# Performance work log

Measured on AMD Instinct MI355X. Metric: run time of the kernel, lower is better.

The kernel has to match this reference:

```python
import jax, jax.numpy as jnp
import numpy as np

N = 65536
R = 9          # num_relations + 1
D_IN = 256
D_HID = 512
D_OUT = 256
N_HIDDEN = 2


def _xavier(key, shape):
    fan_out, fan_in = shape[-2], shape[-1]
    limit = np.sqrt(6.0 / (fan_in + fan_out))
    return jax.random.uniform(key, shape, jnp.float32, -limit, limit)


def setup_inputs() -> dict:
    key = jax.random.key(0)
    ks = jax.random.split(key, 12)
    inp = {
        "x": jax.random.normal(ks[0], (N, D_IN), jnp.float32),
        "edge_attr": jax.random.uniform(ks[1], (N, R), jnp.float32),
    }
    dims = [(D_HID, D_IN)] + [(D_HID, D_HID)] * N_HIDDEN + [(D_OUT, D_HID)]
    for i, (o, ii) in enumerate(dims):
        inp[f"W{i}"] = _xavier(ks[2 + 2 * i], (R, o, ii))
        inp[f"b{i}"] = _xavier(ks[3 + 2 * i], (R, o))
    return inp


def _linear_kg(x, edge_attr, W, b):
    # roi,ni,nr->no : relation-mixed linear per node
    y = jnp.einsum("roi,ni,nr->no", W, x, edge_attr)
    return y + edge_attr @ b


def reference(x, edge_attr, W0, b0, W1, b1, W2, b2, W3, b3):
    y = jax.nn.relu(_linear_kg(x, edge_attr, W0, b0))
    y = jax.nn.relu(_linear_kg(y, edge_attr, W1, b1))
    y = jax.nn.relu(_linear_kg(y, edge_attr, W2, b2))
    y = _linear_kg(y, edge_attr, W3, b3)
    return y
```

## Files before the change

### kernel.cpp

```cpp
#include <hip/hip_runtime.h>
#include <stdint.h>

using f32x4  = __attribute__((ext_vector_type(4))) float;
using bf16x8 = __attribute__((ext_vector_type(8))) __bf16;

#define GLOAD_LDS16(src, dst) __builtin_amdgcn_global_load_lds(                 \
    (const __attribute__((address_space(1))) void*)(src),                      \
    (__attribute__((address_space(3))) void*)(dst), 16, 0, 0)


__global__ void cvt_x_kernel(const float* __restrict__ x, __bf16* __restrict__ out) {
    const int u    = blockIdx.x * 256 + threadIdx.x;
    const int lane = u & 63;
    const int f    = (u >> 6) & 31;
    const int c    = (u >> 11) & 1;
    const int rb   = u >> 12;
    const int row  = rb * 128 + ((f >> 2) << 4) + (lane & 15);
    const int i    = c * 128 + ((f & 3) << 5) + ((lane >> 4) << 3);
    const float4 a = *(const float4*)(x + (size_t)row * 256 + i);
    const float4 b = *(const float4*)(x + (size_t)row * 256 + i + 4);
    bf16x8 pv;
    pv[0] = (__bf16)a.x; pv[1] = (__bf16)a.y; pv[2] = (__bf16)a.z; pv[3] = (__bf16)a.w;
    pv[4] = (__bf16)b.x; pv[5] = (__bf16)b.y; pv[6] = (__bf16)b.z; pv[7] = (__bf16)b.w;
    *(bf16x8*)(out + (size_t)u * 8) = pv;
}

template<int I, int O>
__global__ void prep_w_kernel(const float* __restrict__ W, __bf16* __restrict__ Bt) {
    constexpr int NCH = I >> 7;
    const int u    = blockIdx.x * 256 + threadIdx.x;
    const int r    = blockIdx.y;
    const int nb   = blockIdx.z;
    const int lane = u & 63;
    const int g    = (u >> 6) & 15;
    const int h    = (u >> 10) & 1;
    const int c    = u >> 11;
    const int mi   = g >> 1;
    const int ks   = (h << 1) + (g & 1);
    const int row  = nb * 128 + mi * 16 + (lane & 15);
    const int i    = c * 128 + ks * 32 + ((lane >> 4) << 3);
    const float* src = W + ((size_t)r * O + row) * I + i;
    const float4 a = *(const float4*)src;
    const float4 b = *(const float4*)(src + 4);
    bf16x8 pv;
    pv[0] = (__bf16)a.x; pv[1] = (__bf16)a.y; pv[2] = (__bf16)a.z; pv[3] = (__bf16)a.w;
    pv[4] = (__bf16)b.x; pv[5] = (__bf16)b.y; pv[6] = (__bf16)b.z; pv[7] = (__bf16)b.w;
    *(bf16x8*)(Bt + ((((size_t)nb * 9 + r) * NCH + c) * 2048 + (u & 2047)) * 8) = pv;
}

template<int O>
__global__ void prep_bias_kernel(const float* __restrict__ b, __bf16* __restrict__ BtB) {
    const int u    = blockIdx.x * 256 + threadIdx.x;
    const int nb   = u >> 10;
    const int q    = u & 1023;
    const int lane = q & 63;
    const int f    = q >> 6;
    const int row  = nb * 128 + ((f >> 1) << 4) + (lane & 15);
    const int kb   = ((f & 1) << 5) + ((lane >> 4) << 3);
    bf16x8 pv;
#pragma unroll
    for (int e = 0; e < 8; ++e) {
        const int k = kb + e;
        pv[e] = (k < 9) ? (__bf16)b[(size_t)k * O + row] : (__bf16)0.f;
    }
    *(bf16x8*)(BtB + (size_t)u * 8) = pv;
}

template<int I, int O, bool RELU, bool OUTF32>
__global__ __launch_bounds__(256, 2)
void kg_gemm(const __bf16* __restrict__ A, const float* __restrict__ E,
             const __bf16* __restrict__ Bt, const __bf16* __restrict__ BtB,
             void* __restrict__ Outv) {
    constexpr int NCH = I >> 7;
    constexpr int NBN = O >> 7;
    static_assert((I & 127) == 0 && (O & 127) == 0, "tile divisibility");

    __shared__ __align__(16) char lds[4 * 16384 + 4608];
    float* const ldsE = (float*)(lds + 65536);

    const int tid  = threadIdx.x;
    const int nwg  = gridDim.x;
    const int braw = blockIdx.x;
    const int bid  = (braw & 7) * (nwg >> 3) + (braw >> 3);
    const int rb   = bid / NBN;
    const int nb   = bid % NBN;
    const int bm0  = rb << 7;
    const int bn0  = nb << 7;
    const int lane = tid & 63;
    const int wid  = tid >> 6;
    const int wr   = (wid >> 1) << 6;
    const int wc   = (wid & 1) << 6;
    const int l15  = lane & 15;
    const int lq   = lane >> 4;

    if (tid < 128) {
        const float* e = E + (size_t)(bm0 + tid) * 9;
#pragma unroll
        for (int q = 0; q < 9; ++q) ldsE[q * 128 + tid] = e[q];
    }
    asm volatile("s_waitcnt lgkmcnt(0)" ::: "memory");

    f32x4 acc[4][4];
#pragma unroll
    for (int m = 0; m < 4; ++m)
#pragma unroll
        for (int n = 0; n < 4; ++n)
            acc[m][n] = f32x4{0.f, 0.f, 0.f, 0.f};
    const f32x4 zero4 = {0.f, 0.f, 0.f, 0.f};

    const size_t Abase = (size_t)rb * NCH * 2048;
    const size_t Bbase = (size_t)nb * 9 * NCH * 2048;
    const int afb = (wr >> 4) << 2;
    const int nfb = (wc >> 4) << 1;

    auto stageS = [&](int s, int c) {
        const __bf16* src = Bt + (Bbase + ((size_t)(s >> 1) * NCH + c) * 2048
                                  + (size_t)((s & 1) << 10)) * 8;
        char* dst = lds + ((s & 3) << 14);
#pragma unroll
        for (int it = 0; it < 4; ++it) {
            const int q = it * 256 + tid;
            GLOAD_LDS16(src + (size_t)q * 8, dst + q * 16);
        }
    };

#pragma unroll 1
    for (int c = 0; c < NCH; ++c) {
        __builtin_amdgcn_s_barrier();
        __builtin_amdgcn_sched_barrier(0);
        bf16x8 af[4][4];
        {
            const __bf16* Ab = A + (Abase + (size_t)c * 2048) * 8;
#pragma unroll
            for (int m = 0; m < 4; ++m)
#pragma unroll
                for (int ks = 0; ks < 4; ++ks)
                    af[m][ks] = *(const bf16x8*)(Ab + ((size_t)((afb + (m << 2) + ks) << 6) + lane) * 8);
        }
        stageS(0, c); stageS(1, c); stageS(2, c);

#pragma unroll 1
        for (int r = 0; r < 9; ++r) {
            f32x4 acc2[4][4];
#pragma unroll
            for (int h = 0; h < 2; ++h) {
                const int s = 2 * r + h;
                if (h == 0) {
                    if (r < 8) asm volatile("s_waitcnt vmcnt(8)" ::: "memory");
                    else       asm volatile("s_waitcnt vmcnt(4)" ::: "memory");
                } else {
                    if (r < 8) asm volatile("s_waitcnt vmcnt(8)" ::: "memory");
                    else       asm volatile("s_waitcnt vmcnt(0)" ::: "memory");
                }
                __builtin_amdgcn_s_barrier();
                __builtin_amdgcn_sched_barrier(0);
                if (s + 3 <= 17) stageS(s + 3, c);
                const char* bp = lds + ((s & 3) << 14);
                bf16x8 bv[4][2];
#pragma unroll
                for (int n = 0; n < 4; ++n)
#pragma unroll
                    for (int j = 0; j < 2; ++j)
                        bv[n][j] = *(const bf16x8*)(bp + (((nfb + 2 * n + j) << 6) + lane) * 16);
                __builtin_amdgcn_s_setprio(1);
#pragma unroll
                for (int j = 0; j < 2; ++j)
#pragma unroll
                    for (int m = 0; m < 4; ++m)
#pragma unroll
                        for (int n = 0; n < 4; ++n)
                            acc2[m][n] = __builtin_amdgcn_mfma_f32_16x16x32_bf16(
                                af[m][2 * h + j], bv[n][j],
                                (h == 0 && j == 0) ? zero4 : acc2[m][n], 0, 0, 0);
                __builtin_amdgcn_s_setprio(0);
            }
#pragma unroll
            for (int m = 0; m < 4; ++m) {
                const f32x4 ev = *(const f32x4*)(ldsE + r * 128 + wr + m * 16 + lq * 4);
#pragma unroll
                for (int n = 0; n < 4; ++n)
#pragma unroll
                    for (int j = 0; j < 4; ++j)
                        acc[m][n][j] += ev[j] * acc2[m][n][j];
            }
        }
    }

    __syncthreads();
    {
        char* const bufB = lds;
        char* const bufA = lds + 16384;
#pragma unroll
        for (int rr = 0; rr < 4; ++rr) {
            const int q = rr * 256 + tid;
            GLOAD_LDS16(BtB + ((size_t)nb * 1024 + q) * 8, bufB + q * 16);
        }
#pragma unroll
        for (int rr = 0; rr < 4; ++rr) {
            const int q    = rr * 256 + tid;
            const int ln   = q & 63;
            const int f    = q >> 6;
            const int row  = ((f >> 1) << 4) + (ln & 15);
            const int kb   = ((f & 1) << 5) + ((ln >> 4) << 3);
            bf16x8 pv;
#pragma unroll
            for (int e8 = 0; e8 < 8; ++e8) {
                const int k = kb + e8;
                pv[e8] = (k < 9) ? (__bf16)ldsE[k * 128 + row] : (__bf16)0.f;
            }
            *(bf16x8*)(bufA + q * 16) = pv;
        }
        __syncthreads();
#pragma unroll
        for (int ks = 0; ks < 2; ++ks) {
            bf16x8 av[4], bv[4];
#pragma unroll
            for (int m = 0; m < 4; ++m)
                av[m] = *(const bf16x8*)(bufA + (((((wr >> 4) + m) * 2 + ks) << 6) + lane) * 16);
#pragma unroll
            for (int n = 0; n < 4; ++n)
                bv[n] = *(const bf16x8*)(bufB + (((((wc >> 4) + n) * 2 + ks) << 6) + lane) * 16);
#pragma unroll
            for (int m = 0; m < 4; ++m)
#pragma unroll
                for (int n = 0; n < 4; ++n)
                    acc[m][n] = __builtin_amdgcn_mfma_f32_16x16x32_bf16(
                        av[m], bv[n], acc[m][n], 0, 0, 0);
        }
    }

    if (OUTF32) {
        const int orow0 = bm0 + wr + lq * 4;
        const int ocol0 = bn0 + wc + l15;
#pragma unroll
        for (int m = 0; m < 4; ++m)
#pragma unroll
            for (int n = 0; n < 4; ++n)
#pragma unroll
                for (int j = 0; j < 4; ++j) {
                    float v = acc[m][n][j];
                    if (RELU) v = fmaxf(v, 0.f);
                    ((float*)Outv)[(size_t)(orow0 + m * 16 + j) * O + (ocol0 + n * 16)] = v;
                }
    } else {
        constexpr int NCHn = O >> 7;
        __bf16* outp = (__bf16*)Outv;
#pragma unroll
        for (int m = 0; m < 4; ++m) {
#pragma unroll
            for (int n = 0; n < 4; ++n) {
                const int col  = bn0 + wc + n * 16 + l15;
                const int c2   = col >> 7;
                const int f2   = (((wr >> 4) + m) << 2) + ((col >> 5) & 3);
                const int ln2  = ((col >> 3) & 3) * 16 + lq * 4;
                const size_t base =
                    (((size_t)rb * NCHn + c2) * 2048 + f2 * 64 + ln2) * 8 + (col & 7);
#pragma unroll
                for (int j = 0; j < 4; ++j) {
                    float v = acc[m][n][j];
                    if (RELU) v = fmaxf(v, 0.f);
                    outp[base + (size_t)j * 8] = (__bf16)v;
                }
            }
        }
    }
}

extern "C" void kernel_launch(void* const* d_in, const int* in_sizes, int n_in,
                              void* d_out, int out_size, void* d_ws, size_t ws_size,
                              hipStream_t stream) {
    const float* x  = (const float*)d_in[0];
    const float* E  = (const float*)d_in[1];
    const float* W0 = (const float*)d_in[2];
    const float* b0 = (const float*)d_in[3];
    const float* W1 = (const float*)d_in[4];
    const float* b1 = (const float*)d_in[5];
    const float* W2 = (const float*)d_in[6];
    const float* b2 = (const float*)d_in[7];
    const float* W3 = (const float*)d_in[8];
    const float* b3 = (const float*)d_in[9];

    char* ws = (char*)d_ws;
    const size_t actBytes = (size_t)65536 * 512 * 2;
    __bf16* actA = (__bf16*)ws;
    __bf16* actB = (__bf16*)(ws + actBytes);
    char* p = ws + 2 * actBytes;
    __bf16* Bt0 = (__bf16*)p; p += (size_t)4 * 9 * 2 * 2048 * 16;
    __bf16* Bt1 = (__bf16*)p; p += (size_t)4 * 9 * 4 * 2048 * 16;
    __bf16* Bt2 = (__bf16*)p; p += (size_t)4 * 9 * 4 * 2048 * 16;
    __bf16* Bt3 = (__bf16*)p; p += (size_t)2 * 9 * 4 * 2048 * 16;
    __bf16* BtB0 = (__bf16*)p; p += (size_t)4 * 1024 * 16;
    __bf16* BtB1 = (__bf16*)p; p += (size_t)4 * 1024 * 16;
    __bf16* BtB2 = (__bf16*)p; p += (size_t)4 * 1024 * 16;
    __bf16* BtB3 = (__bf16*)p; p += (size_t)2 * 1024 * 16;
    if (ws_size < (size_t)(p - ws)) return;

    cvt_x_kernel<<<dim3(8192), dim3(256), 0, stream>>>(x, actA);
    prep_w_kernel<256, 512><<<dim3(16, 9, 4), dim3(256), 0, stream>>>(W0, Bt0);
    prep_w_kernel<512, 512><<<dim3(32, 9, 4), dim3(256), 0, stream>>>(W1, Bt1);
    prep_w_kernel<512, 512><<<dim3(32, 9, 4), dim3(256), 0, stream>>>(W2, Bt2);
    prep_w_kernel<512, 256><<<dim3(32, 9, 2), dim3(256), 0, stream>>>(W3, Bt3);
    prep_bias_kernel<512><<<dim3(16), dim3(256), 0, stream>>>(b0, BtB0);
    prep_bias_kernel<512><<<dim3(16), dim3(256), 0, stream>>>(b1, BtB1);
    prep_bias_kernel<512><<<dim3(16), dim3(256), 0, stream>>>(b2, BtB2);
    prep_bias_kernel<256><<<dim3(8),  dim3(256), 0, stream>>>(b3, BtB3);

    kg_gemm<256, 512, true,  false><<<dim3(2048), dim3(256), 0, stream>>>(actA, E, Bt0, BtB0, actB);
    kg_gemm<512, 512, true,  false><<<dim3(2048), dim3(256), 0, stream>>>(actB, E, Bt1, BtB1, actA);
    kg_gemm<512, 512, true,  false><<<dim3(2048), dim3(256), 0, stream>>>(actA, E, Bt2, BtB2, actB);
    kg_gemm<512, 256, false, true ><<<dim3(1024), dim3(256), 0, stream>>>(actB, E, Bt3, BtB3, d_out);
}
```

Before: 847.9 us.

## Swap loop order to relation-outer, K-chunk-inner with double-buffered A fragments

Reorders the main GEMM loop so relations are the outer loop and K half-chunks the inner loop. Each relation's partial sum now covers the full K dimension before it is scaled by its edge weight, so the E-scaling epilogue runs 9 times instead of 9*NCH times. A fragments are reloaded per phase into ping-pong register buffers instead of being held for a whole chunk, which adds repeated global loads of A across relations. The B staging pipeline is now continuous across relations, and at the tail it issues redundant stages so the vmcnt accounting stays uniform.

New measurement: 2.140 ms. 152% more time.

```diff
diff --git a/kernel.cpp b/kernel.cpp
--- a/kernel.cpp
+++ b/kernel.cpp
@@ -71,8 +71,9 @@
 void kg_gemm(const __bf16* __restrict__ A, const float* __restrict__ E,
              const __bf16* __restrict__ Bt, const __bf16* __restrict__ BtB,
              void* __restrict__ Outv) {
-    constexpr int NCH = I >> 7;
-    constexpr int NBN = O >> 7;
+    constexpr int NCH  = I >> 7;
+    constexpr int NBN  = O >> 7;
+    constexpr int PHR  = 2 * NCH;
     static_assert((I & 127) == 0 && (O & 127) == 0, "tile divisibility");
 
     __shared__ __align__(16) char lds[4 * 16384 + 4608];
@@ -99,6 +100,7 @@
         for (int q = 0; q < 9; ++q) ldsE[q * 128 + tid] = e[q];
     }
     asm volatile("s_waitcnt lgkmcnt(0)" ::: "memory");
+    __builtin_amdgcn_s_barrier();
 
     f32x4 acc[4][4];
 #pragma unroll
@@ -108,81 +110,79 @@
             acc[m][n] = f32x4{0.f, 0.f, 0.f, 0.f};
     const f32x4 zero4 = {0.f, 0.f, 0.f, 0.f};
 
-    const size_t Abase = (size_t)rb * NCH * 2048;
     const size_t Bbase = (size_t)nb * 9 * NCH * 2048;
+    const __bf16* Arb  = A + (size_t)rb * NCH * 2048 * 8;
     const int afb = (wr >> 4) << 2;
     const int nfb = (wc >> 4) << 1;
 
-    auto stageS = [&](int s, int c) {
-        const __bf16* src = Bt + (Bbase + ((size_t)(s >> 1) * NCH + c) * 2048
-                                  + (size_t)((s & 1) << 10)) * 8;
-        char* dst = lds + ((s & 3) << 14);
+    auto stageB = [&](int rr, int ch) {
+        const __bf16* src = Bt + (Bbase + ((size_t)rr * NCH + (ch >> 1)) * 2048
+                                  + (size_t)((ch & 1) << 10)) * 8;
+        char* dst = lds + ((((rr * PHR) + ch) & 3) << 14);
 #pragma unroll
         for (int it = 0; it < 4; ++it) {
             const int q = it * 256 + tid;
             GLOAD_LDS16(src + (size_t)q * 8, dst + q * 16);
         }
     };
+    auto loadAF = [&](bf16x8 (&af)[4][2], int ch) {
+        const __bf16* Ab = Arb + (size_t)(ch >> 1) * 2048 * 8;
+        const int h = ch & 1;
+#pragma unroll
+        for (int m = 0; m < 4; ++m)
+#pragma unroll
+            for (int j = 0; j < 2; ++j)
+                af[m][j] = *(const bf16x8*)(Ab + ((size_t)((afb + (m << 2) + (h << 1) + j) << 6) + lane) * 8);
+    };
+
+    bf16x8 afA[4][2], afB[4][2];
+    loadAF(afA, 0);
+    stageB(0, 0); stageB(0, 1); stageB(0, 2);
 
 #pragma unroll 1
-    for (int c = 0; c < NCH; ++c) {
-        __builtin_amdgcn_s_barrier();
-        __builtin_amdgcn_sched_barrier(0);
-        bf16x8 af[4][4];
-        {
-            const __bf16* Ab = A + (Abase + (size_t)c * 2048) * 8;
-#pragma unroll
-            for (int m = 0; m < 4; ++m)
-#pragma unroll
-                for (int ks = 0; ks < 4; ++ks)
-                    af[m][ks] = *(const bf16x8*)(Ab + ((size_t)((afb + (m << 2) + ks) << 6) + lane) * 8);
-        }
-        stageS(0, c); stageS(1, c); stageS(2, c);
-
-#pragma unroll 1
-        for (int r = 0; r < 9; ++r) {
-            f32x4 acc2[4][4];
-#pragma unroll
-            for (int h = 0; h < 2; ++h) {
-                const int s = 2 * r + h;
-                if (h == 0) {
-                    if (r < 8) asm volatile("s_waitcnt vmcnt(8)" ::: "memory");
-                    else       asm volatile("s_waitcnt vmcnt(4)" ::: "memory");
-                } else {
-                    if (r < 8) asm volatile("s_waitcnt vmcnt(8)" ::: "memory");
-                    else       asm volatile("s_waitcnt vmcnt(0)" ::: "memory");
-                }
-                __builtin_amdgcn_s_barrier();
-                __builtin_amdgcn_sched_barrier(0);
-                if (s + 3 <= 17) stageS(s + 3, c);
-                const char* bp = lds + ((s & 3) << 14);
-                bf16x8 bv[4][2];
-#pragma unroll
-                for (int n = 0; n < 4; ++n)
-#pragma unroll
-                    for (int j = 0; j < 2; ++j)
-                        bv[n][j] = *(const bf16x8*)(bp + (((nfb + 2 * n + j) << 6) + lane) * 16);
-                __builtin_amdgcn_s_setprio(1);
+    for (int r = 0; r < 9; ++r) {
+        f32x4 acc2[4][4];
+#pragma unroll
+        for (int pc = 0; pc < PHR; ++pc) {
+            if (pc == 0 && r == 0) asm volatile("s_waitcnt vmcnt(8)" ::: "memory");
+            else                   asm volatile("s_waitcnt vmcnt(4)" ::: "memory");
+            __builtin_amdgcn_s_barrier();
+            __builtin_amdgcn_sched_barrier(0);
+            if (pc & 1) loadAF(afA, (pc + 1) & (PHR - 1));
+            else        loadAF(afB, (pc + 1) & (PHR - 1));
+            {
+                int rr = r + ((pc + 3) / PHR);
+                int ch = (pc + 3) & (PHR - 1);
+                if (rr > 8) { rr = 8; ch = PHR - 1; }
+                stageB(rr, ch);
+            }
+            const char* bp = lds + ((pc & 3) << 14);
+            bf16x8 bv[4][2];
+#pragma unroll
+            for (int n = 0; n < 4; ++n)
 #pragma unroll
                 for (int j = 0; j < 2; ++j)
-#pragma unroll
-                    for (int m = 0; m < 4; ++m)
-#pragma unroll
-                        for (int n = 0; n < 4; ++n)
-                            acc2[m][n] = __builtin_amdgcn_mfma_f32_16x16x32_bf16(
-                                af[m][2 * h + j], bv[n][j],
-                                (h == 0 && j == 0) ? zero4 : acc2[m][n], 0, 0, 0);
-                __builtin_amdgcn_s_setprio(0);
-            }
-#pragma unroll
-            for (int m = 0; m < 4; ++m) {
-                const f32x4 ev = *(const f32x4*)(ldsE + r * 128 + wr + m * 16 + lq * 4);
-#pragma unroll
-                for (int n = 0; n < 4; ++n)
-#pragma unroll
-                    for (int j = 0; j < 4; ++j)
-                        acc[m][n][j] += ev[j] * acc2[m][n][j];
-            }
+                    bv[n][j] = *(const bf16x8*)(bp + (((nfb + 2 * n + j) << 6) + lane) * 16);
+            __builtin_amdgcn_s_setprio(1);
+#pragma unroll
+            for (int j = 0; j < 2; ++j)
+#pragma unroll
+                for (int m = 0; m < 4; ++m)
+#pragma unroll
+                    for (int n = 0; n < 4; ++n)
+                        acc2[m][n] = __builtin_amdgcn_mfma_f32_16x16x32_bf16(
+                            (pc & 1) ? afB[m][j] : afA[m][j], bv[n][j],
+                            (pc == 0 && j == 0) ? zero4 : acc2[m][n], 0, 0, 0);
+            __builtin_amdgcn_s_setprio(0);
+        }
+#pragma unroll
+        for (int m = 0; m < 4; ++m) {
+            const f32x4 ev = *(const f32x4*)(ldsE + r * 128 + wr + m * 16 + lq * 4);
+#pragma unroll
+            for (int n = 0; n < 4; ++n)
+#pragma unroll
+                for (int j = 0; j < 4; ++j)
+                    acc[m][n][j] += ev[j] * acc2[m][n][j];
         }
     }
 
```

## Give each wave private LDS staging of its B slice to drop block barriers

Applied to the files above, without the earlier changes.

Each wave now loads only the 64-column slice of B that it consumes into its own 16KB LDS region, double-buffered by half-step. This removes the per-stage workgroup s_barrier calls and the cross-wave staging of B. The next relation's B is prefetched across chunk boundaries, and the A fragment loads move inside the first step so they overlap with in-flight B loads. The trade-off is that waves sharing a column range now fetch duplicate B data from global memory, and the waitcnt accounting depends on per-wave issue order.

After: 970.8 us. +14.5%, slower.

```diff
diff --git a/kernel.cpp b/kernel.cpp
--- a/kernel.cpp
+++ b/kernel.cpp
@@ -75,7 +75,7 @@
     constexpr int NBN = O >> 7;
     static_assert((I & 127) == 0 && (O & 127) == 0, "tile divisibility");
 
-    __shared__ __align__(16) char lds[4 * 16384 + 4608];
+    __shared__ __align__(16) char lds[65536 + 4608];
     float* const ldsE = (float*)(lds + 65536);
 
     const int tid  = threadIdx.x;
@@ -99,6 +99,7 @@
         for (int q = 0; q < 9; ++q) ldsE[q * 128 + tid] = e[q];
     }
     asm volatile("s_waitcnt lgkmcnt(0)" ::: "memory");
+    __builtin_amdgcn_s_barrier();
 
     f32x4 acc[4][4];
 #pragma unroll
@@ -108,60 +109,62 @@
             acc[m][n] = f32x4{0.f, 0.f, 0.f, 0.f};
     const f32x4 zero4 = {0.f, 0.f, 0.f, 0.f};
 
-    const size_t Abase = (size_t)rb * NCH * 2048;
     const size_t Bbase = (size_t)nb * 9 * NCH * 2048;
+    const __bf16* Arb  = A + (size_t)rb * NCH * 2048 * 8;
     const int afb = (wr >> 4) << 2;
-    const int nfb = (wc >> 4) << 1;
-
-    auto stageS = [&](int s, int c) {
-        const __bf16* src = Bt + (Bbase + ((size_t)(s >> 1) * NCH + c) * 2048
-                                  + (size_t)((s & 1) << 10)) * 8;
-        char* dst = lds + ((s & 3) << 14);
-#pragma unroll
-        for (int it = 0; it < 4; ++it) {
-            const int q = it * 256 + tid;
+    const int g0  = (wc >> 4) << 1;
+    char* const wlds = lds + (wid << 14);
+
+    auto stageW = [&](int r2, int c2, int h2) {
+        const __bf16* src = Bt + (Bbase + ((size_t)r2 * NCH + c2) * 2048
+                                  + (h2 << 10) + (g0 << 6)) * 8;
+        char* dst = wlds + (h2 << 13);
+#pragma unroll
+        for (int it = 0; it < 8; ++it) {
+            const int q = it * 64 + lane;
             GLOAD_LDS16(src + (size_t)q * 8, dst + q * 16);
         }
     };
+
+    bf16x8 af[4][4];
+    stageW(0, 0, 0); stageW(0, 0, 1);
 
 #pragma unroll 1
     for (int c = 0; c < NCH; ++c) {
-        __builtin_amdgcn_s_barrier();
-        __builtin_amdgcn_sched_barrier(0);
-        bf16x8 af[4][4];
-        {
-            const __bf16* Ab = A + (Abase + (size_t)c * 2048) * 8;
-#pragma unroll
-            for (int m = 0; m < 4; ++m)
-#pragma unroll
-                for (int ks = 0; ks < 4; ++ks)
-                    af[m][ks] = *(const bf16x8*)(Ab + ((size_t)((afb + (m << 2) + ks) << 6) + lane) * 8);
-        }
-        stageS(0, c); stageS(1, c); stageS(2, c);
-
 #pragma unroll 1
         for (int r = 0; r < 9; ++r) {
             f32x4 acc2[4][4];
 #pragma unroll
             for (int h = 0; h < 2; ++h) {
-                const int s = 2 * r + h;
-                if (h == 0) {
-                    if (r < 8) asm volatile("s_waitcnt vmcnt(8)" ::: "memory");
-                    else       asm volatile("s_waitcnt vmcnt(4)" ::: "memory");
+                const bool first = (r == 0) && (h == 0);
+                const bool lastC = (c == NCH - 1);
+                if (first) {
+                    const __bf16* Ab = Arb + (size_t)c * 2048 * 8;
+#pragma unroll
+                    for (int m = 0; m < 4; ++m)
+#pragma unroll
+                        for (int ks = 0; ks < 4; ++ks)
+                            af[m][ks] = *(const bf16x8*)(Ab + ((size_t)((afb + (m << 2) + ks) << 6) + lane) * 8);
+                    asm volatile("s_waitcnt vmcnt(24)" ::: "memory");
+                } else if (lastC && r == 8 && h == 1) {
+                    asm volatile("s_waitcnt vmcnt(0)" ::: "memory");
                 } else {
-                    if (r < 8) asm volatile("s_waitcnt vmcnt(8)" ::: "memory");
-                    else       asm volatile("s_waitcnt vmcnt(0)" ::: "memory");
+                    asm volatile("s_waitcnt vmcnt(8)" ::: "memory");
                 }
-                __builtin_amdgcn_s_barrier();
                 __builtin_amdgcn_sched_barrier(0);
-                if (s + 3 <= 17) stageS(s + 3, c);
-                const char* bp = lds + ((s & 3) << 14);
+                const char* bp = wlds + (h << 13);
                 bf16x8 bv[4][2];
 #pragma unroll
                 for (int n = 0; n < 4; ++n)
 #pragma unroll
                     for (int j = 0; j < 2; ++j)
-                        bv[n][j] = *(const bf16x8*)(bp + (((nfb + 2 * n + j) << 6) + lane) * 16);
+                        bv[n][j] = *(const bf16x8*)(bp + ((((n << 1) + j) << 6) + lane) * 16);
+                asm volatile("s_waitcnt lgkmcnt(0)" ::: "memory");
+                __builtin_amdgcn_sched_barrier(0);
+                if (!(lastC && r == 8))
+                    stageW((r < 8) ? r + 1 : 0, (r < 8) ? c : c + 1, h);
+                if (first) asm volatile("s_waitcnt vmcnt(8)" ::: "memory");
+                __builtin_amdgcn_sched_barrier(0);
                 __builtin_amdgcn_s_setprio(1);
 #pragma unroll
                 for (int j = 0; j < 2; ++j)
@@ -170,7 +173,7 @@
 #pragma unroll
                         for (int n = 0; n < 4; ++n)
                             acc2[m][n] = __builtin_amdgcn_mfma_f32_16x16x32_bf16(
-                                af[m][2 * h + j], bv[n][j],
+                                af[m][(h << 1) + j], bv[n][j],
                                 (h == 0 && j == 0) ? zero4 : acc2[m][n], 0, 0, 0);
                 __builtin_amdgcn_s_setprio(0);
             }
```

## Halve N tile to 64 columns and raise occupancy to three blocks per CU

Applied to the files above, without the earlier changes.

Shrinks each workgroup's output tile from 128x128 to 128x64, halving the per-stage B tiles in LDS and the accumulator registers, and doubles the grid. Launch bounds go from 2 to 3 blocks per CU to raise occupancy. The per-relation scaling is now applied right after each half-K MFMA pair instead of holding a full temporary accumulator. In exchange, A fragments are reloaded twice as often per output, and the edge-weight FMAs now run every half-step.

After: 2.440 ms. 2.88x slower.

```diff
diff --git a/kernel.cpp b/kernel.cpp
--- a/kernel.cpp
+++ b/kernel.cpp
@@ -67,16 +67,16 @@
 }
 
 template<int I, int O, bool RELU, bool OUTF32>
-__global__ __launch_bounds__(256, 2)
+__global__ __launch_bounds__(256, 3)
 void kg_gemm(const __bf16* __restrict__ A, const float* __restrict__ E,
              const __bf16* __restrict__ Bt, const __bf16* __restrict__ BtB,
              void* __restrict__ Outv) {
     constexpr int NCH = I >> 7;
-    constexpr int NBN = O >> 7;
+    constexpr int NBN = O >> 6;
     static_assert((I & 127) == 0 && (O & 127) == 0, "tile divisibility");
 
-    __shared__ __align__(16) char lds[4 * 16384 + 4608];
-    float* const ldsE = (float*)(lds + 65536);
+    __shared__ __align__(16) char lds[4 * 8192 + 4608];
+    float* const ldsE = (float*)(lds + 32768);
 
     const int tid  = threadIdx.x;
     const int nwg  = gridDim.x;
@@ -85,13 +85,16 @@
     const int rb   = bid / NBN;
     const int nb   = bid % NBN;
     const int bm0  = rb << 7;
-    const int bn0  = nb << 7;
+    const int bn0  = nb << 6;
+    const int nb128 = nb >> 1;
+    const int G0u  = (nb & 1) << 9;
     const int lane = tid & 63;
     const int wid  = tid >> 6;
     const int wr   = (wid >> 1) << 6;
-    const int wc   = (wid & 1) << 6;
+    const int wc   = (wid & 1) << 5;
     const int l15  = lane & 15;
     const int lq   = lane >> 4;
+    const int nfb2 = (wid & 1) << 1;
 
     if (tid < 128) {
         const float* e = E + (size_t)(bm0 + tid) * 9;
@@ -100,25 +103,24 @@
     }
     asm volatile("s_waitcnt lgkmcnt(0)" ::: "memory");
 
-    f32x4 acc[4][4];
+    f32x4 acc[4][2];
 #pragma unroll
     for (int m = 0; m < 4; ++m)
 #pragma unroll
-        for (int n = 0; n < 4; ++n)
+        for (int n = 0; n < 2; ++n)
             acc[m][n] = f32x4{0.f, 0.f, 0.f, 0.f};
     const f32x4 zero4 = {0.f, 0.f, 0.f, 0.f};
 
     const size_t Abase = (size_t)rb * NCH * 2048;
-    const size_t Bbase = (size_t)nb * 9 * NCH * 2048;
+    const size_t Bbase = (size_t)nb128 * 9 * NCH * 2048;
     const int afb = (wr >> 4) << 2;
-    const int nfb = (wc >> 4) << 1;
 
     auto stageS = [&](int s, int c) {
         const __bf16* src = Bt + (Bbase + ((size_t)(s >> 1) * NCH + c) * 2048
-                                  + (size_t)((s & 1) << 10)) * 8;
-        char* dst = lds + ((s & 3) << 14);
-#pragma unroll
-        for (int it = 0; it < 4; ++it) {
+                                  + (size_t)(((s & 1) << 10) + G0u)) * 8;
+        char* dst = lds + ((s & 3) << 13);
+#pragma unroll
+        for (int it = 0; it < 2; ++it) {
             const int q = it * 256 + tid;
             GLOAD_LDS16(src + (size_t)q * 8, dst + q * 16);
         }
@@ -141,47 +143,48 @@
 
 #pragma unroll 1
         for (int r = 0; r < 9; ++r) {
-            f32x4 acc2[4][4];
 #pragma unroll
             for (int h = 0; h < 2; ++h) {
-                const int s = 2 * r + h;
                 if (h == 0) {
-                    if (r < 8) asm volatile("s_waitcnt vmcnt(8)" ::: "memory");
-                    else       asm volatile("s_waitcnt vmcnt(4)" ::: "memory");
+                    if (r < 8) asm volatile("s_waitcnt vmcnt(4)" ::: "memory");
+                    else       asm volatile("s_waitcnt vmcnt(2)" ::: "memory");
                 } else {
-                    if (r < 8) asm volatile("s_waitcnt vmcnt(8)" ::: "memory");
+                    if (r < 8) asm volatile("s_waitcnt vmcnt(4)" ::: "memory");
                     else       asm volatile("s_waitcnt vmcnt(0)" ::: "memory");
                 }
                 __builtin_amdgcn_s_barrier();
                 __builtin_amdgcn_sched_barrier(0);
+                const int s = 2 * r + h;
                 if (s + 3 <= 17) stageS(s + 3, c);
-                const char* bp = lds + ((s & 3) << 14);
-                bf16x8 bv[4][2];
-#pragma unroll
-                for (int n = 0; n < 4; ++n)
+                const char* bp = lds + ((s & 3) << 13);
+                bf16x8 bv[2][2];
+#pragma unroll
+                for (int n = 0; n < 2; ++n)
 #pragma unroll
                     for (int j = 0; j < 2; ++j)
-                        bv[n][j] = *(const bf16x8*)(bp + (((nfb + 2 * n + j) << 6) + lane) * 16);
-                __builtin_amdgcn_s_setprio(1);
-#pragma unroll
-                for (int j = 0; j < 2; ++j)
-#pragma unroll
-                    for (int m = 0; m < 4; ++m)
-#pragma unroll
-                        for (int n = 0; n < 4; ++n)
-                            acc2[m][n] = __builtin_amdgcn_mfma_f32_16x16x32_bf16(
-                                af[m][2 * h + j], bv[n][j],
-                                (h == 0 && j == 0) ? zero4 : acc2[m][n], 0, 0, 0);
-                __builtin_amdgcn_s_setprio(0);
-            }
-#pragma unroll
-            for (int m = 0; m < 4; ++m) {
-                const f32x4 ev = *(const f32x4*)(ldsE + r * 128 + wr + m * 16 + lq * 4);
-#pragma unroll
-                for (int n = 0; n < 4; ++n)
-#pragma unroll
-                    for (int j = 0; j < 4; ++j)
-                        acc[m][n][j] += ev[j] * acc2[m][n][j];
+                        bv[n][j] = *(const bf16x8*)(bp + ((((nfb2 + n) * 2 + j) << 6) + lane) * 16);
+                f32x4 ev0 = *(const f32x4*)(ldsE + r * 128 + wr + 0  + lq * 4);
+                f32x4 ev1 = *(const f32x4*)(ldsE + r * 128 + wr + 16 + lq * 4);
+                f32x4 ev2 = *(const f32x4*)(ldsE + r * 128 + wr + 32 + lq * 4);
+                f32x4 ev3 = *(const f32x4*)(ldsE + r * 128 + wr + 48 + lq * 4);
+#pragma unroll
+                for (int n = 0; n < 2; ++n) {
+                    f32x4 t0 = __builtin_amdgcn_mfma_f32_16x16x32_bf16(af[0][2*h], bv[n][0], zero4, 0, 0, 0);
+                    f32x4 t1 = __builtin_amdgcn_mfma_f32_16x16x32_bf16(af[1][2*h], bv[n][0], zero4, 0, 0, 0);
+                    f32x4 t2 = __builtin_amdgcn_mfma_f32_16x16x32_bf16(af[2][2*h], bv[n][0], zero4, 0, 0, 0);
+                    f32x4 t3 = __builtin_amdgcn_mfma_f32_16x16x32_bf16(af[3][2*h], bv[n][0], zero4, 0, 0, 0);
+                    t0 = __builtin_amdgcn_mfma_f32_16x16x32_bf16(af[0][2*h+1], bv[n][1], t0, 0, 0, 0);
+                    t1 = __builtin_amdgcn_mfma_f32_16x16x32_bf16(af[1][2*h+1], bv[n][1], t1, 0, 0, 0);
+                    t2 = __builtin_amdgcn_mfma_f32_16x16x32_bf16(af[2][2*h+1], bv[n][1], t2, 0, 0, 0);
+                    t3 = __builtin_amdgcn_mfma_f32_16x16x32_bf16(af[3][2*h+1], bv[n][1], t3, 0, 0, 0);
+#pragma unroll
+                    for (int j = 0; j < 4; ++j) {
+                        acc[0][n][j] += ev0[j] * t0[j];
+                        acc[1][n][j] += ev1[j] * t1[j];
+                        acc[2][n][j] += ev2[j] * t2[j];
+                        acc[3][n][j] += ev3[j] * t3[j];
+                    }
+                }
             }
         }
     }
@@ -189,11 +192,11 @@
     __syncthreads();
     {
         char* const bufB = lds;
-        char* const bufA = lds + 16384;
-#pragma unroll
-        for (int rr = 0; rr < 4; ++rr) {
-            const int q = rr * 256 + tid;
-            GLOAD_LDS16(BtB + ((size_t)nb * 1024 + q) * 8, bufB + q * 16);
+        char* const bufA = lds + 8192;
+#pragma unroll
+        for (int it = 0; it < 2; ++it) {
+            const int q = it * 256 + tid;
+            GLOAD_LDS16(BtB + ((size_t)nb128 * 1024 + G0u + q) * 8, bufB + q * 16);
         }
 #pragma unroll
         for (int rr = 0; rr < 4; ++rr) {
@@ -213,17 +216,17 @@
         __syncthreads();
 #pragma unroll
         for (int ks = 0; ks < 2; ++ks) {
-            bf16x8 av[4], bv[4];
+            bf16x8 av[4], bv[2];
 #pragma unroll
             for (int m = 0; m < 4; ++m)
                 av[m] = *(const bf16x8*)(bufA + (((((wr >> 4) + m) * 2 + ks) << 6) + lane) * 16);
 #pragma unroll
-            for (int n = 0; n < 4; ++n)
-                bv[n] = *(const bf16x8*)(bufB + (((((wc >> 4) + n) * 2 + ks) << 6) + lane) * 16);
+            for (int n = 0; n < 2; ++n)
+                bv[n] = *(const bf16x8*)(bufB + ((((nfb2 + n) * 2 + ks) << 6) + lane) * 16);
 #pragma unroll
             for (int m = 0; m < 4; ++m)
 #pragma unroll
-                for (int n = 0; n < 4; ++n)
+                for (int n = 0; n < 2; ++n)
                     acc[m][n] = __builtin_amdgcn_mfma_f32_16x16x32_bf16(
                         av[m], bv[n], acc[m][n], 0, 0, 0);
         }
@@ -235,7 +238,7 @@
 #pragma unroll
         for (int m = 0; m < 4; ++m)
 #pragma unroll
-            for (int n = 0; n < 4; ++n)
+            for (int n = 0; n < 2; ++n)
 #pragma unroll
                 for (int j = 0; j < 4; ++j) {
                     float v = acc[m][n][j];
@@ -248,7 +251,7 @@
 #pragma unroll
         for (int m = 0; m < 4; ++m) {
 #pragma unroll
-            for (int n = 0; n < 4; ++n) {
+            for (int n = 0; n < 2; ++n) {
                 const int col  = bn0 + wc + n * 16 + l15;
                 const int c2   = col >> 7;
                 const int f2   = (((wr >> 4) + m) << 2) + ((col >> 5) & 3);
@@ -305,8 +308,8 @@
     prep_bias_kernel<512><<<dim3(16), dim3(256), 0, stream>>>(b2, BtB2);
     prep_bias_kernel<256><<<dim3(8),  dim3(256), 0, stream>>>(b3, BtB3);
 
-    kg_gemm<256, 512, true,  false><<<dim3(2048), dim3(256), 0, stream>>>(actA, E, Bt0, BtB0, actB);
-    kg_gemm<512, 512, true,  false><<<dim3(2048), dim3(256), 0, stream>>>(actB, E, Bt1, BtB1, actA);
-    kg_gemm<512, 512, true,  false><<<dim3(2048), dim3(256), 0, stream>>>(actA, E, Bt2, BtB2, actB);
-    kg_gemm<512, 256, false, true ><<<dim3(1024), dim3(256), 0, stream>>>(actB, E, Bt3, BtB3, d_out);
-}
+    kg_gemm<256, 512, true,  false><<<dim3(4096), dim3(256), 0, stream>>>(actA, E, Bt0, BtB0, actB);
+    kg_gemm<512, 512, true,  false><<<dim3(4096), dim3(256), 0, stream>>>(actB, E, Bt1, BtB1, actA);
+    kg_gemm<512, 512, true,  false><<<dim3(4096), dim3(256), 0, stream>>>(actA, E, Bt2, BtB2, actB);
+    kg_gemm<512, 256, false, true ><<<dim3(2048), dim3(256), 0, stream>>>(actB, E, Bt3, BtB3, d_out);
+}
```
